# Kernel tuning notes

Hardware: AMD Instinct MI355X
Metric: run time of the kernel (lower is better)

The kernel has to match this reference:

```python
import jax, jax.numpy as jnp
import numpy as np

B, T, H = 4096, 512, 512
GATE = 2 + H  # concat([x(1), h(H), mask(1)])


def setup_inputs() -> dict:
    key = jax.random.key(0)
    ks = jax.random.split(key, 20)
    s = 1.0 / np.sqrt(GATE)
    inp = {
        "x": jax.random.normal(ks[0], (B, T), jnp.float32),
        "x_last": jax.random.normal(ks[1], (B, T), jnp.float32),
        "interval": jax.random.uniform(ks[2], (B, T), jnp.float32),
        "mask": (jax.random.uniform(ks[3], (B, T)) > 0.3).astype(jnp.float32),
        # gamma decay layers
        "Wgx": jax.random.normal(ks[4], (1, 1), jnp.float32),
        "bgx": jnp.zeros((1,), jnp.float32),
        "Wgh": jax.random.normal(ks[5], (H, 1), jnp.float32),
        "bgh": jnp.zeros((H,), jnp.float32),
        # gate layers: Linear(GATE, H)
        "Wz": jax.random.normal(ks[6], (H, GATE), jnp.float32) * s,
        "bz": jnp.zeros((H,), jnp.float32),
        "Wr": jax.random.normal(ks[7], (H, GATE), jnp.float32) * s,
        "br": jnp.zeros((H,), jnp.float32),
        "Wh": jax.random.normal(ks[8], (H, GATE), jnp.float32) * s,
        "bh": jnp.zeros((H,), jnp.float32),
        # output head Linear(H, 1)
        "Wo": jax.random.normal(ks[9], (1, H), jnp.float32) / np.sqrt(H),
        "bo": jnp.zeros((1,), jnp.float32),
    }
    return inp


def reference(x, x_last, interval, mask, Wgx, bgx, Wgh, bgh,
              Wz, bz, Wr, br, Wh, bh, Wo, bo):
    # x, x_last, interval, mask: [B, T]; feature dim is 1 after unsqueeze
    x3 = x[..., None]            # [B, T, 1]
    xl3 = x_last[..., None]
    it3 = interval[..., None]
    m3 = mask[..., None]
    # mean(x*m, dim=1) * T / sum(m, dim=1) == sum(x*m)/sum(m)
    x_mean = jnp.sum(x3 * m3, axis=1) / jnp.sum(m3, axis=1)  # [B, 1]

    h0 = jnp.zeros((x.shape[0], Wz.shape[0]), x.dtype)
    # time-major stacks for scan: [T, B, 1]
    xs = (jnp.swapaxes(x3, 0, 1), jnp.swapaxes(xl3, 0, 1),
          jnp.swapaxes(m3, 0, 1), jnp.swapaxes(it3, 0, 1))

    def step(h, ts):
        xt, xl, mt, it = ts  # each [B, 1]
        gamma_x = jnp.exp(-jax.nn.relu(it @ Wgx.T + bgx))   # [B, 1]
        gamma_h = jnp.exp(-jax.nn.relu(it @ Wgh.T + bgh))   # [B, H]
        xi = mt * xt + (1.0 - mt) * (gamma_x * xl + (1.0 - gamma_x) * x_mean)
        h = gamma_h * h
        comb = jnp.concatenate([xi, h, mt], axis=1)          # [B, GATE]
        z = jax.nn.sigmoid(comb @ Wz.T + bz)
        r = jax.nn.sigmoid(comb @ Wr.T + br)
        comb_r = jnp.concatenate([xi, r * h, mt], axis=1)
        h_tilde = jnp.tanh(comb_r @ Wh.T + bh)
        h = (1.0 - z) * h + z * h_tilde
        return h, None

    h, _ = jax.lax.scan(step, h0, xs)
    return jax.nn.sigmoid(h @ Wo.T + bo)  # [B, 1]
```

## Files before the change

### kernel.cpp

```cpp
#include <hip/hip_runtime.h>
#include <stdint.h>

#define T_LEN 512
#define H_DIM 512
#define B_TOT 4096
#define GATE_D 514
#define CLUSTERS 16
#define RANKS 16
#define CROWS 256
#define OWNC 32
#define NTHR 512
#define HLS 33
#define RLS 34
#define BARPAD 64

typedef short s16x8 __attribute__((ext_vector_type(8)));
typedef float f32x4 __attribute__((ext_vector_type(4)));

__device__ __forceinline__ ushort f2bf(float f) {
    uint32_t u = __builtin_bit_cast(uint32_t, f);
    u += 0x7FFF + ((u >> 16) & 1);
    return (ushort)(u >> 16);
}
__device__ __forceinline__ float sigmoid_f(float x) {
    return 1.0f / (1.0f + __expf(-x));
}
__device__ __forceinline__ float tanh_f(float x) {
    float ax = fabsf(x);
    float e  = __expf(2.0f * ax);
    float t  = 1.0f - 2.0f / (e + 1.0f);
    return copysignf(t, x);
}
__device__ __forceinline__ void vm0() {
    asm volatile("s_waitcnt vmcnt(0)" ::: "memory");
}

__global__ void k_xmean(const float* __restrict__ x, const float* __restrict__ m,
                        float* __restrict__ xmean) {
    int b = blockIdx.x;
    int l = threadIdx.x;
    const float* xr = x + (size_t)b * T_LEN;
    const float* mr = m + (size_t)b * T_LEN;
    float sx = 0.f, sm = 0.f;
    #pragma unroll
    for (int i = 0; i < T_LEN / 64; ++i) {
        float mv = mr[l + i * 64];
        sx += xr[l + i * 64] * mv;
        sm += mv;
    }
    for (int off = 32; off; off >>= 1) {
        sx += __shfl_down(sx, off);
        sm += __shfl_down(sm, off);
    }
    if (l == 0) xmean[b] = sx / sm;
}

__global__ void k_init(unsigned int* barc) {
    int i = threadIdx.x + blockIdx.x * blockDim.x;
    if (i < CLUSTERS * BARPAD) barc[i] = 0u;
}

__device__ __forceinline__ void bar_slow(unsigned int* cnt, unsigned int target) {
    vm0();
    __syncthreads();
    if (threadIdx.x == 0) {
        __builtin_amdgcn_fence(__ATOMIC_RELEASE, "agent");
        __hip_atomic_fetch_add(cnt, 1u, __ATOMIC_RELAXED, __HIP_MEMORY_SCOPE_AGENT);
        while (__hip_atomic_load(cnt, __ATOMIC_RELAXED, __HIP_MEMORY_SCOPE_AGENT) < target)
            __builtin_amdgcn_s_sleep(1);
        __builtin_amdgcn_fence(__ATOMIC_ACQUIRE, "agent");
    }
    __syncthreads();
}

__device__ __forceinline__ void bar_fast(unsigned int* cnt, unsigned int target) {
    vm0();
    __syncthreads();
    if (threadIdx.x == 0) {
        __hip_atomic_fetch_add(cnt, 1u, __ATOMIC_RELAXED, __HIP_MEMORY_SCOPE_AGENT);
        while (__hip_atomic_load(cnt, __ATOMIC_RELAXED, __HIP_MEMORY_SCOPE_AGENT) < target)
            __builtin_amdgcn_s_sleep(1);
        asm volatile("buffer_inv" ::: "memory");
        vm0();
    }
    __syncthreads();
}

__global__ __launch_bounds__(NTHR, 2) void k_grud(
    const float* __restrict__ x,   const float* __restrict__ xl,
    const float* __restrict__ itv, const float* __restrict__ msk,
    const float* __restrict__ Wgx, const float* __restrict__ bgx,
    const float* __restrict__ Wgh, const float* __restrict__ bgh,
    const float* __restrict__ Wz,  const float* __restrict__ bz,
    const float* __restrict__ Wr,  const float* __restrict__ br,
    const float* __restrict__ Wh,  const float* __restrict__ bh,
    const float* __restrict__ Wo,  const float* __restrict__ bo,
    const float* __restrict__ xmean,
    ushort* __restrict__ hdx, ushort* __restrict__ rhx,
    float* __restrict__ osum, unsigned int* __restrict__ barc,
    float* __restrict__ out)
{
    __shared__ ushort wfrag[96 * 512];
    __shared__ float  h_lds[CROWS * HLS];
    __shared__ ushort rhd_s[CROWS * RLS];
    __shared__ float  xi_s[CROWS], mts_s[CROWS], its_s[CROWS];
    __shared__ float4 epi_s[96];
    __shared__ float2 ghb_s[OWNC];
    __shared__ unsigned int flag_s;

    const int tid = threadIdx.x;
    const int b   = blockIdx.x;
    const int cluster = (b & 7) * 2 + ((b >> 3) >> 4);
    const int rank    = (b >> 3) & 15;
    const int wv = tid >> 6, l = tid & 63;
    const int colb = l & 15, qg = l >> 4;
    const int r0 = cluster * CROWS;

    unsigned int* cnt     = barc + cluster * BARPAD;
    unsigned int* xcd_arr = cnt + 16;
    ushort* hdc = hdx + (size_t)cluster * CROWS * H_DIM;
    ushort* rhc = rhx + (size_t)cluster * CROWS * H_DIM;
    const s16x8* WF = (const s16x8*)wfrag;
    const s16x8* HD = (const s16x8*)hdc;
    const s16x8* RH = (const s16x8*)rhc;

    for (int i = tid; i < CROWS * HLS; i += NTHR) h_lds[i] = 0.f;
    for (int s = tid; s < 96 * 64; s += NTHR) {
        int fi = s >> 6, ln = s & 63;
        int g = fi >> 5, nt = (fi >> 4) & 1, kt = fi & 15;
        const float* W = (g == 0) ? Wz : (g == 1) ? Wr : Wh;
        int colg = rank * OWNC + nt * 16 + (ln & 15);
        int c0 = 1 + kt * 32 + (ln >> 4) * 8;
        ushort tb[8];
        #pragma unroll
        for (int j = 0; j < 8; ++j) tb[j] = f2bf(W[(size_t)colg * GATE_D + c0 + j]);
        *(s16x8*)&wfrag[s * 8] = *(s16x8*)tb;
    }
    for (int i = tid; i < 96; i += NTHR) {
        int g = i >> 5, c = i & 31;
        const float* W  = (g == 0) ? Wz : (g == 1) ? Wr : Wh;
        const float* bb = (g == 0) ? bz : (g == 1) ? br : bh;
        int colg = rank * OWNC + c;
        epi_s[i] = make_float4(bb[colg], W[(size_t)colg * GATE_D],
                               W[(size_t)colg * GATE_D + GATE_D - 1], 0.f);
    }
    if (tid < OWNC) ghb_s[tid] = make_float2(Wgh[rank * OWNC + tid], bgh[rank * OWNC + tid]);
    const float wgx = Wgx[0], bgx0 = bgx[0];

    if (tid == 0) {
        unsigned int myxcc;
        asm volatile("s_getreg_b32 %0, hwreg(HW_REG_XCC_ID)" : "=s"(myxcc));
        xcd_arr[rank] = myxcc;
    }
    unsigned int ep = 1;
    bar_slow(cnt, RANKS * ep);
    if (tid == 0) {
        unsigned int x0 = xcd_arr[0], same = 1;
        #pragma unroll
        for (int rk = 1; rk < RANKS; ++rk) same &= (xcd_arr[rk] == x0) ? 1u : 0u;
        flag_s = same;
    }
    __syncthreads();
    const bool fastc = (flag_s != 0);

    float zq[2][2][4];

    for (int t = 0; t < T_LEN; ++t) {
        if (tid < CROWS) {
            size_t idx = (size_t)(r0 + tid) * T_LEN + t;
            float xv = x[idx], xlv = xl[idx], iv = itv[idx], mv = msk[idx];
            float gx = __expf(-fmaxf(iv * wgx + bgx0, 0.f));
            xi_s[tid]  = mv * xv + (1.f - mv) * (gx * xlv + (1.f - gx) * xmean[r0 + tid]);
            mts_s[tid] = mv;
            its_s[tid] = iv;
        }
        __syncthreads();

        #pragma unroll
        for (int i = 0; i < 2; ++i) {
            int s = tid + i * NTHR;
            int mt = s >> 6, ln = s & 63;
            int row = mt * 16 + (ln & 15);
            int c0 = (ln >> 4) * 8;
            float it = its_s[row];
            float hv[8]; ushort tb[8];
            #pragma unroll
            for (int j = 0; j < 8; ++j) {
                float2 gb = ghb_s[c0 + j];
                float g  = __expf(-fmaxf(it * gb.x + gb.y, 0.f));
                float hd = h_lds[row * HLS + c0 + j] * g;
                hv[j] = hd; tb[j] = f2bf(hd);
            }
            #pragma unroll
            for (int j = 0; j < 8; ++j) h_lds[row * HLS + c0 + j] = hv[j];
            *(s16x8*)&hdc[((mt * 16 + rank) * 64 + ln) * 8] = *(s16x8*)tb;
        }
        ++ep;
        if (fastc) bar_fast(cnt, RANKS * ep); else bar_slow(cnt, RANKS * ep);

        f32x4 accz[2][2], accr[2][2];
        #pragma unroll
        for (int mt = 0; mt < 2; ++mt)
            #pragma unroll
            for (int nt = 0; nt < 2; ++nt) { accz[mt][nt] = (f32x4){0,0,0,0}; accr[mt][nt] = (f32x4){0,0,0,0}; }
        #pragma unroll
        for (int kt = 0; kt < 16; ++kt) {
            s16x8 a0 = HD[((2 * wv    ) * 16 + kt) * 64 + l];
            s16x8 a1 = HD[((2 * wv + 1) * 16 + kt) * 64 + l];
            #pragma unroll
            for (int nt = 0; nt < 2; ++nt) {
                s16x8 bz_ = WF[(     nt * 16 + kt) * 64 + l];
                s16x8 br_ = WF[(32 + nt * 16 + kt) * 64 + l];
                accz[0][nt] = __builtin_amdgcn_mfma_f32_16x16x32_bf16(a0, bz_, accz[0][nt], 0, 0, 0);
                accz[1][nt] = __builtin_amdgcn_mfma_f32_16x16x32_bf16(a1, bz_, accz[1][nt], 0, 0, 0);
                accr[0][nt] = __builtin_amdgcn_mfma_f32_16x16x32_bf16(a0, br_, accr[0][nt], 0, 0, 0);
                accr[1][nt] = __builtin_amdgcn_mfma_f32_16x16x32_bf16(a1, br_, accr[1][nt], 0, 0, 0);
            }
        }
        #pragma unroll
        for (int mt = 0; mt < 2; ++mt) {
            #pragma unroll
            for (int nt = 0; nt < 2; ++nt) {
                int c = nt * 16 + colb;
                float4 ez = epi_s[c];
                float4 er = epi_s[32 + c];
                #pragma unroll
                for (int q = 0; q < 4; ++q) {
                    int row = wv * 32 + mt * 16 + qg * 4 + q;
                    float xiv = xi_s[row], mtv = mts_s[row];
                    zq[mt][nt][q] = sigmoid_f(accz[mt][nt][q] + ez.x + xiv * ez.y + mtv * ez.z);
                    float rr = sigmoid_f(accr[mt][nt][q] + er.x + xiv * er.y + mtv * er.z);
                    float hd = h_lds[row * HLS + c];
                    rhd_s[row * RLS + c] = f2bf(rr * hd);
                }
            }
        }
        __syncthreads();
        #pragma unroll
        for (int i = 0; i < 2; ++i) {
            int s = tid + i * NTHR;
            int mt = s >> 6, ln = s & 63;
            int row = mt * 16 + (ln & 15);
            int c0 = (ln >> 4) * 8;
            ushort tb[8];
            #pragma unroll
            for (int j = 0; j < 8; ++j) tb[j] = rhd_s[row * RLS + c0 + j];
            *(s16x8*)&rhc[((mt * 16 + rank) * 64 + ln) * 8] = *(s16x8*)tb;
        }
        ++ep;
        if (fastc) bar_fast(cnt, RANKS * ep); else bar_slow(cnt, RANKS * ep);

        f32x4 acc2[2][2];
        #pragma unroll
        for (int mt = 0; mt < 2; ++mt)
            #pragma unroll
            for (int nt = 0; nt < 2; ++nt) acc2[mt][nt] = (f32x4){0,0,0,0};
        #pragma unroll
        for (int kt = 0; kt < 16; ++kt) {
            s16x8 a0 = RH[((2 * wv    ) * 16 + kt) * 64 + l];
            s16x8 a1 = RH[((2 * wv + 1) * 16 + kt) * 64 + l];
            #pragma unroll
            for (int nt = 0; nt < 2; ++nt) {
                s16x8 bh_ = WF[(64 + nt * 16 + kt) * 64 + l];
                acc2[0][nt] = __builtin_amdgcn_mfma_f32_16x16x32_bf16(a0, bh_, acc2[0][nt], 0, 0, 0);
                acc2[1][nt] = __builtin_amdgcn_mfma_f32_16x16x32_bf16(a1, bh_, acc2[1][nt], 0, 0, 0);
            }
        }
        #pragma unroll
        for (int mt = 0; mt < 2; ++mt) {
            #pragma unroll
            for (int nt = 0; nt < 2; ++nt) {
                int c = nt * 16 + colb;
                float4 eh = epi_s[64 + c];
                #pragma unroll
                for (int q = 0; q < 4; ++q) {
                    int row = wv * 32 + mt * 16 + qg * 4 + q;
                    float ht = tanh_f(acc2[mt][nt][q] + eh.x + xi_s[row] * eh.y + mts_s[row] * eh.z);
                    float hd = h_lds[row * HLS + c];
                    h_lds[row * HLS + c] = hd + zq[mt][nt][q] * (ht - hd);
                }
            }
        }
        __syncthreads();
    }

    if (tid < CROWS) {
        float s = 0.f;
        #pragma unroll
        for (int c = 0; c < OWNC; ++c) s += h_lds[tid * HLS + c] * Wo[rank * OWNC + c];
        osum[(size_t)(r0 + tid) * RANKS + rank] = s;
    }
    ++ep;
    if (fastc) bar_fast(cnt, RANKS * ep); else bar_slow(cnt, RANKS * ep);
    if (rank == 0 && tid < CROWS) {
        float s = 0.f;
        #pragma unroll
        for (int rk = 0; rk < RANKS; ++rk) s += osum[(size_t)(r0 + tid) * RANKS + rk];
        out[r0 + tid] = sigmoid_f(s + bo[0]);
    }
}

extern "C" void kernel_launch(void* const* d_in, const int* in_sizes, int n_in,
                              void* d_out, int out_size, void* d_ws, size_t ws_size,
                              hipStream_t stream) {
    const float* x    = (const float*)d_in[0];
    const float* xl   = (const float*)d_in[1];
    const float* itv  = (const float*)d_in[2];
    const float* msk  = (const float*)d_in[3];
    const float* Wgx  = (const float*)d_in[4];
    const float* bgx  = (const float*)d_in[5];
    const float* Wgh  = (const float*)d_in[6];
    const float* bgh  = (const float*)d_in[7];
    const float* Wz   = (const float*)d_in[8];
    const float* bz   = (const float*)d_in[9];
    const float* Wr   = (const float*)d_in[10];
    const float* br   = (const float*)d_in[11];
    const float* Wh   = (const float*)d_in[12];
    const float* bh   = (const float*)d_in[13];
    const float* Wo   = (const float*)d_in[14];
    const float* bo   = (const float*)d_in[15];

    char* ws = (char*)d_ws;
    float*        xmean = (float*)ws;
    unsigned int* barc  = (unsigned int*)(ws + 16384);
    float*        osum  = (float*)(ws + 16384 + 4096);
    ushort*       hdx   = (ushort*)(ws + 16384 + 4096 + 262144);
    ushort*       rhx   = (ushort*)(ws + 16384 + 4096 + 262144 + 4194304);

    k_init<<<1, 1024, 0, stream>>>(barc);
    k_xmean<<<B_TOT, 64, 0, stream>>>(x, msk, xmean);
    k_grud<<<CLUSTERS * RANKS, NTHR, 0, stream>>>(
        x, xl, itv, msk, Wgx, bgx, Wgh, bgh,
        Wz, bz, Wr, br, Wh, bh, Wo, bo,
        xmean, hdx, rhx, osum, barc, (float*)d_out);
}
```

Baseline: 6.982 ms.

## Keep hidden state in registers, fuse decay into update, overlap input prefetch with barrier

Moves each lane's hidden-state slice from an LDS array into registers. The next step's gamma_h decay and bf16 publish of h are folded into the end-of-step update, which removes the separate decay pass and one syncthreads per step. The per-step input loads are double-buffered and issued between the barrier arrive and its spin-wait, and half of the Wh fragments move into registers to free LDS. The cost is higher register pressure under the 2-block launch bound, plus a more intricate hand-written barrier sequence that must stay correct.

New measurement: 11.32 ms. 62.1% more time.

```diff
diff --git a/kernel.cpp b/kernel.cpp
--- a/kernel.cpp
+++ b/kernel.cpp
@@ -10,8 +10,6 @@
 #define CROWS 256
 #define OWNC 32
 #define NTHR 512
-#define HLS 33
-#define RLS 34
 #define BARPAD 64
 
 typedef short s16x8 __attribute__((ext_vector_type(8)));
@@ -100,10 +98,9 @@
     float* __restrict__ osum, unsigned int* __restrict__ barc,
     float* __restrict__ out)
 {
-    __shared__ ushort wfrag[96 * 512];
-    __shared__ float  h_lds[CROWS * HLS];
-    __shared__ ushort rhd_s[CROWS * RLS];
-    __shared__ float  xi_s[CROWS], mts_s[CROWS], its_s[CROWS];
+    __shared__ ushort wfrag[80 * 512];
+    __shared__ ushort stage[16 * 512];
+    __shared__ float  xi_s[2][CROWS], mts_s[2][CROWS], its_s[2][CROWS];
     __shared__ float4 epi_s[96];
     __shared__ float2 ghb_s[OWNC];
     __shared__ unsigned int flag_s;
@@ -124,18 +121,30 @@
     const s16x8* HD = (const s16x8*)hdc;
     const s16x8* RH = (const s16x8*)rhc;
 
-    for (int i = tid; i < CROWS * HLS; i += NTHR) h_lds[i] = 0.f;
-    for (int s = tid; s < 96 * 64; s += NTHR) {
+    for (int s = tid; s < 80 * 64; s += NTHR) {
         int fi = s >> 6, ln = s & 63;
-        int g = fi >> 5, nt = (fi >> 4) & 1, kt = fi & 15;
-        const float* W = (g == 0) ? Wz : (g == 1) ? Wr : Wh;
-        int colg = rank * OWNC + nt * 16 + (ln & 15);
+        const float* W; int kt, ntl;
+        if (fi < 64) { int g = fi >> 5; W = g ? Wr : Wz; int id = fi & 31; ntl = id >> 4; kt = id & 15; }
+        else         { int id = fi - 64; W = Wh; ntl = id >> 3; kt = 8 + (id & 7); }
+        int colg = rank * OWNC + ntl * 16 + (ln & 15);
         int c0 = 1 + kt * 32 + (ln >> 4) * 8;
         ushort tb[8];
         #pragma unroll
         for (int j = 0; j < 8; ++j) tb[j] = f2bf(W[(size_t)colg * GATE_D + c0 + j]);
         *(s16x8*)&wfrag[s * 8] = *(s16x8*)tb;
     }
+    s16x8 whreg[16];
+    #pragma unroll
+    for (int nt = 0; nt < 2; ++nt)
+        #pragma unroll
+        for (int kt = 0; kt < 8; ++kt) {
+            int colg = rank * OWNC + nt * 16 + (l & 15);
+            int c0 = 1 + kt * 32 + (l >> 4) * 8;
+            ushort tb[8];
+            #pragma unroll
+            for (int j = 0; j < 8; ++j) tb[j] = f2bf(Wh[(size_t)colg * GATE_D + c0 + j]);
+            whreg[nt * 8 + kt] = *(s16x8*)tb;
+        }
     for (int i = tid; i < 96; i += NTHR) {
         int g = i >> 5, c = i & 31;
         const float* W  = (g == 0) ? Wz : (g == 1) ? Wr : Wh;
@@ -147,6 +156,23 @@
     if (tid < OWNC) ghb_s[tid] = make_float2(Wgh[rank * OWNC + tid], bgh[rank * OWNC + tid]);
     const float wgx = Wgx[0], bgx0 = bgx[0];
 
+    #pragma unroll
+    for (int i = 0; i < 2; ++i) {
+        int s = tid + i * NTHR;
+        *(s16x8*)((char*)hdc + ((size_t)(s >> 6) * 1024 + (size_t)rank * 64 + (s & 63)) * 16) = (s16x8){0,0,0,0,0,0,0,0};
+    }
+
+    float xmv = 0.f;
+    if (tid < CROWS) {
+        xmv = xmean[r0 + tid];
+        size_t idx = (size_t)(r0 + tid) * T_LEN;
+        float xv = x[idx], xlv = xl[idx], iv = itv[idx], mv = msk[idx];
+        float gx = __expf(-fmaxf(iv * wgx + bgx0, 0.f));
+        xi_s[0][tid]  = mv * xv + (1.f - mv) * (gx * xlv + (1.f - gx) * xmv);
+        mts_s[0][tid] = mv;
+        its_s[0][tid] = iv;
+    }
+
     if (tid == 0) {
         unsigned int myxcc;
         asm volatile("s_getreg_b32 %0, hwreg(HW_REG_XCC_ID)" : "=s"(myxcc));
@@ -163,40 +189,17 @@
     __syncthreads();
     const bool fastc = (flag_s != 0);
 
+    float hdq[2][2][4];
+    #pragma unroll
+    for (int mt = 0; mt < 2; ++mt)
+        #pragma unroll
+        for (int nt = 0; nt < 2; ++nt)
+            #pragma unroll
+            for (int q = 0; q < 4; ++q) hdq[mt][nt][q] = 0.f;
     float zq[2][2][4];
 
     for (int t = 0; t < T_LEN; ++t) {
-        if (tid < CROWS) {
-            size_t idx = (size_t)(r0 + tid) * T_LEN + t;
-            float xv = x[idx], xlv = xl[idx], iv = itv[idx], mv = msk[idx];
-            float gx = __expf(-fmaxf(iv * wgx + bgx0, 0.f));
-            xi_s[tid]  = mv * xv + (1.f - mv) * (gx * xlv + (1.f - gx) * xmean[r0 + tid]);
-            mts_s[tid] = mv;
-            its_s[tid] = iv;
-        }
-        __syncthreads();
-
-        #pragma unroll
-        for (int i = 0; i < 2; ++i) {
-            int s = tid + i * NTHR;
-            int mt = s >> 6, ln = s & 63;
-            int row = mt * 16 + (ln & 15);
-            int c0 = (ln >> 4) * 8;
-            float it = its_s[row];
-            float hv[8]; ushort tb[8];
-            #pragma unroll
-            for (int j = 0; j < 8; ++j) {
-                float2 gb = ghb_s[c0 + j];
-                float g  = __expf(-fmaxf(it * gb.x + gb.y, 0.f));
-                float hd = h_lds[row * HLS + c0 + j] * g;
-                hv[j] = hd; tb[j] = f2bf(hd);
-            }
-            #pragma unroll
-            for (int j = 0; j < 8; ++j) h_lds[row * HLS + c0 + j] = hv[j];
-            *(s16x8*)&hdc[((mt * 16 + rank) * 64 + ln) * 8] = *(s16x8*)tb;
-        }
-        ++ep;
-        if (fastc) bar_fast(cnt, RANKS * ep); else bar_slow(cnt, RANKS * ep);
+        const int sl = t & 1;
 
         f32x4 accz[2][2], accr[2][2];
         #pragma unroll
@@ -224,14 +227,15 @@
                 int c = nt * 16 + colb;
                 float4 ez = epi_s[c];
                 float4 er = epi_s[32 + c];
+                int grp = (c >> 3) & 3, jj = c & 7;
                 #pragma unroll
                 for (int q = 0; q < 4; ++q) {
                     int row = wv * 32 + mt * 16 + qg * 4 + q;
-                    float xiv = xi_s[row], mtv = mts_s[row];
+                    float xiv = xi_s[sl][row], mtv = mts_s[sl][row];
                     zq[mt][nt][q] = sigmoid_f(accz[mt][nt][q] + ez.x + xiv * ez.y + mtv * ez.z);
                     float rr = sigmoid_f(accr[mt][nt][q] + er.x + xiv * er.y + mtv * er.z);
-                    float hd = h_lds[row * HLS + c];
-                    rhd_s[row * RLS + c] = f2bf(rr * hd);
+                    stage[(((2 * wv + mt) * 64) + (qg * 4 + q) + grp * 16) * 8 + jj] =
+                        f2bf(rr * hdq[mt][nt][q]);
                 }
             }
         }
@@ -239,16 +243,35 @@
         #pragma unroll
         for (int i = 0; i < 2; ++i) {
             int s = tid + i * NTHR;
-            int mt = s >> 6, ln = s & 63;
-            int row = mt * 16 + (ln & 15);
-            int c0 = (ln >> 4) * 8;
-            ushort tb[8];
-            #pragma unroll
-            for (int j = 0; j < 8; ++j) tb[j] = rhd_s[row * RLS + c0 + j];
-            *(s16x8*)&rhc[((mt * 16 + rank) * 64 + ln) * 8] = *(s16x8*)tb;
+            *(s16x8*)((char*)rhc + ((size_t)(s >> 6) * 1024 + (size_t)rank * 64 + (s & 63)) * 16) =
+                *(const s16x8*)&stage[s * 8];
         }
         ++ep;
-        if (fastc) bar_fast(cnt, RANKS * ep); else bar_slow(cnt, RANKS * ep);
+        {
+            unsigned int target = RANKS * ep;
+            vm0();
+            __syncthreads();
+            if (tid == 0) {
+                if (!fastc) __builtin_amdgcn_fence(__ATOMIC_RELEASE, "agent");
+                __hip_atomic_fetch_add(cnt, 1u, __ATOMIC_RELAXED, __HIP_MEMORY_SCOPE_AGENT);
+            }
+            if (tid < CROWS && t + 1 < T_LEN) {
+                size_t idx = (size_t)(r0 + tid) * T_LEN + t + 1;
+                float xv = x[idx], xlv = xl[idx], iv = itv[idx], mv = msk[idx];
+                float gx = __expf(-fmaxf(iv * wgx + bgx0, 0.f));
+                int s2 = sl ^ 1;
+                xi_s[s2][tid]  = mv * xv + (1.f - mv) * (gx * xlv + (1.f - gx) * xmv);
+                mts_s[s2][tid] = mv;
+                its_s[s2][tid] = iv;
+            }
+            if (tid == 0) {
+                while (__hip_atomic_load(cnt, __ATOMIC_RELAXED, __HIP_MEMORY_SCOPE_AGENT) < target)
+                    __builtin_amdgcn_s_sleep(1);
+                if (fastc) { asm volatile("buffer_inv" ::: "memory"); vm0(); }
+                else __builtin_amdgcn_fence(__ATOMIC_ACQUIRE, "agent");
+            }
+            __syncthreads();
+        }
 
         f32x4 acc2[2][2];
         #pragma unroll
@@ -261,34 +284,62 @@
             s16x8 a1 = RH[((2 * wv + 1) * 16 + kt) * 64 + l];
             #pragma unroll
             for (int nt = 0; nt < 2; ++nt) {
-                s16x8 bh_ = WF[(64 + nt * 16 + kt) * 64 + l];
+                s16x8 bh_ = (kt < 8) ? whreg[nt * 8 + kt]
+                                     : WF[(64 + nt * 8 + (kt - 8)) * 64 + l];
                 acc2[0][nt] = __builtin_amdgcn_mfma_f32_16x16x32_bf16(a0, bh_, acc2[0][nt], 0, 0, 0);
                 acc2[1][nt] = __builtin_amdgcn_mfma_f32_16x16x32_bf16(a1, bh_, acc2[1][nt], 0, 0, 0);
             }
         }
+        const bool last = (t + 1 == T_LEN);
         #pragma unroll
         for (int mt = 0; mt < 2; ++mt) {
             #pragma unroll
             for (int nt = 0; nt < 2; ++nt) {
                 int c = nt * 16 + colb;
                 float4 eh = epi_s[64 + c];
+                float2 gb = ghb_s[c];
+                int grp = (c >> 3) & 3, jj = c & 7;
                 #pragma unroll
                 for (int q = 0; q < 4; ++q) {
                     int row = wv * 32 + mt * 16 + qg * 4 + q;
-                    float ht = tanh_f(acc2[mt][nt][q] + eh.x + xi_s[row] * eh.y + mts_s[row] * eh.z);
-                    float hd = h_lds[row * HLS + c];
-                    h_lds[row * HLS + c] = hd + zq[mt][nt][q] * (ht - hd);
+                    float ht = tanh_f(acc2[mt][nt][q] + eh.x + xi_s[sl][row] * eh.y + mts_s[sl][row] * eh.z);
+                    float hd = hdq[mt][nt][q];
+                    float hn = hd + zq[mt][nt][q] * (ht - hd);
+                    float g  = last ? 1.f : __expf(-fmaxf(its_s[sl ^ 1][row] * gb.x + gb.y, 0.f));
+                    float hdn = hn * g;
+                    hdq[mt][nt][q] = hdn;
+                    if (!last)
+                        stage[(((2 * wv + mt) * 64) + (qg * 4 + q) + grp * 16) * 8 + jj] = f2bf(hdn);
                 }
             }
         }
         __syncthreads();
-    }
-
-    if (tid < CROWS) {
-        float s = 0.f;
-        #pragma unroll
-        for (int c = 0; c < OWNC; ++c) s += h_lds[tid * HLS + c] * Wo[rank * OWNC + c];
-        osum[(size_t)(r0 + tid) * RANKS + rank] = s;
+        if (!last) {
+            #pragma unroll
+            for (int i = 0; i < 2; ++i) {
+                int s = tid + i * NTHR;
+                *(s16x8*)((char*)hdc + ((size_t)(s >> 6) * 1024 + (size_t)rank * 64 + (s & 63)) * 16) =
+                    *(const s16x8*)&stage[s * 8];
+            }
+        }
+        ++ep;
+        if (fastc) bar_fast(cnt, RANKS * ep); else bar_slow(cnt, RANKS * ep);
+    }
+
+    {
+        float wo0 = Wo[rank * OWNC + colb];
+        float wo1 = Wo[rank * OWNC + 16 + colb];
+        #pragma unroll
+        for (int mt = 0; mt < 2; ++mt) {
+            #pragma unroll
+            for (int q = 0; q < 4; ++q) {
+                int row = wv * 32 + mt * 16 + qg * 4 + q;
+                float p = hdq[mt][0][q] * wo0 + hdq[mt][1][q] * wo1;
+                #pragma unroll
+                for (int off = 1; off < 16; off <<= 1) p += __shfl_xor(p, off);
+                if (colb == 0) osum[(size_t)(r0 + row) * RANKS + rank] = p;
+            }
+        }
     }
     ++ep;
     if (fastc) bar_fast(cnt, RANKS * ep); else bar_slow(cnt, RANKS * ep);
```
